# Kernel tuning notes

Hardware: AMD Instinct MI355X
Metric: run time of the kernel (lower is better)

Reference implementation:

```python
import jax, jax.numpy as jnp
import numpy as np
jax.config.update("jax_enable_x64", True)

N_ITER = 5
B, N = 64, 128

_C1 = jnp.uint64(0x9E3779B97F4A7C15)
_C2 = jnp.uint64(0xBF58476D1CE4E5B9)
_C3 = jnp.uint64(0x94D049BB133111EB)
_SALT = jnp.uint64(0xD1B54A32D192ED03)


def _mix(x):
    # splitmix64 finalizer: a bijection on uint64 -> preserves label equality classes
    z = x + _C1
    z = (z ^ (z >> jnp.uint64(30))) * _C2
    z = (z ^ (z >> jnp.uint64(27))) * _C3
    return z ^ (z >> jnp.uint64(31))


def setup_inputs() -> dict:
    key = jax.random.key(0)
    k1, k2 = jax.random.split(key)
    u = jax.random.uniform(k1, (B, N, N))
    adj = jnp.where(u < 0.06, 1.0, 0.0).astype(jnp.float32)
    adj = jnp.maximum(adj, jnp.transpose(adj, (0, 2, 1)))  # symmetric
    eye = jnp.eye(N, dtype=jnp.float32)
    adj = adj * (1.0 - eye)  # no self loops
    labels = jax.random.randint(k2, (B, N), 0, 10, dtype=jnp.int32)
    return {"adj": adj, "labels": labels}


def _kernel_contrib(h):
    # h: [B, N] uint64 labels. K[i,j] = #{(u,v): label_u == label_v}
    L = h.reshape(-1)                                   # [T]
    eq = (L[:, None] == L[None, :]).astype(jnp.float32)  # [T, T]
    return eq.reshape(B, N, B, N).sum(axis=(1, 3))       # [B, B]


def reference(adj, labels):
    adj_u = (adj > 0.5).astype(jnp.uint64)        # [B, N, N]
    h = _mix(labels.astype(jnp.uint64))           # initial labels (bijective relabel)
    K = _kernel_contrib(h)
    for _ in range(N_ITER):
        # commutative multiset hash of neighbor labels
        nsum = jnp.einsum('bij,bj->bi', adj_u, _mix(h ^ _SALT))
        # combine own label with neighbor multiset -> WL relabel
        h = _mix(_mix(h) + nsum)
        K = K + _kernel_contrib(h)
    d = jnp.sqrt(jnp.diag(K))
    return K / (d[:, None] * d[None, :])
```

## Files before the change

kernel.cpp:

```cpp
#include <hip/hip_runtime.h>

typedef unsigned long long u64;
typedef unsigned int u32;

#define NB 64
#define NN 128
#define NITER 5
#define NGEN 6
#define SALT 0xD1B54A32D192ED03ULL
#define NPAIR_OFF (NB*(NB-1)/2)
#define TSLOTS 256

__device__ __forceinline__ u64 mix64(u64 x) {
    u64 z = x + 0x9E3779B97F4A7C15ULL;
    z = (z ^ (z >> 30)) * 0xBF58476D1CE4E5B9ULL;
    z = (z ^ (z >> 27)) * 0x94D049BB133111EBULL;
    return z ^ (z >> 31);
}

__global__ __launch_bounds__(512) void wl_iter(const float* __restrict__ adj,
                                               const int* __restrict__ labels,
                                               u64* __restrict__ hgen,
                                               u32* __restrict__ KdiagU,
                                               float* __restrict__ out) {
    const int b = blockIdx.x;
    const int t = threadIdx.x;
    const int u = t & 127;
    const int q = t >> 7;

    __shared__ u64 gsh[NN];
    __shared__ u64 psum[3][NN];

    const float* rowp = adj + ((size_t)b * NN + u) * NN + q * 32;
    u32 m = 0;
    #pragma unroll
    for (int k = 0; k < 8; ++k) {
        const float4 v = *(const float4*)(rowp + 4 * k);
        m |= (v.x > 0.5f ? 1u : 0u) << (4 * k);
        m |= (v.y > 0.5f ? 1u : 0u) << (4 * k + 1);
        m |= (v.z > 0.5f ? 1u : 0u) << (4 * k + 2);
        m |= (v.w > 0.5f ? 1u : 0u) << (4 * k + 3);
    }

    u64 h = 0;
    if (q == 0) {
        h = mix64((u64)(u32)labels[b * NN + u]);
        hgen[((size_t)b * NGEN) * NN + u] = h;
        if (u == 0) out[b * NB + b] = 1.0f;
        if (u == 1) KdiagU[b] = 0u;
    }

    for (int it = 0; it < NITER; ++it) {
        if (q == 0) gsh[u] = mix64(h ^ SALT);
        __syncthreads();
        u64 s = 0;
        {
            u32 mm = m;
            const u64* gp = gsh + q * 32;
            while (mm) { int j = __builtin_ctz(mm); mm &= mm - 1; s += gp[j]; }
        }
        if (q) psum[q - 1][u] = s;
        __syncthreads();
        if (q == 0) {
            h = mix64(mix64(h) + s + psum[0][u] + psum[1][u] + psum[2][u]);
            hgen[((size_t)b * NGEN + (it + 1)) * NN + u] = h;
        }
    }
}

__global__ __launch_bounds__(128) void wl_tables(const u64* __restrict__ hgen,
                                                 u64* __restrict__ keysg,
                                                 u32* __restrict__ cntsg,
                                                 u32* __restrict__ KdiagU) {
    const int bg = blockIdx.x;
    const int t = threadIdx.x;

    __shared__ u64 keys[TSLOTS];
    __shared__ u32 cnts[TSLOTS];
    keys[t] = 0ULL; keys[t + 128] = 0ULL;
    cnts[t] = 0u;   cnts[t + 128] = 0u;
    __syncthreads();

    const u64 h = hgen[(size_t)bg * NN + t];
    u32 s = (u32)h & (TSLOTS - 1);
    for (;;) {
        u64 old = atomicCAS((unsigned long long*)&keys[s], 0ULL, h);
        if (old == 0ULL || old == h) { atomicAdd(&cnts[s], 1u); break; }
        s = (s + 1) & (TSLOTS - 1);
    }
    __syncthreads();

    u32 acc;
    {
        const u64 k0 = keys[t], k1 = keys[t + 128];
        const u32 c0 = cnts[t], c1 = cnts[t + 128];
        keysg[(size_t)bg * TSLOTS + t]       = k0;
        keysg[(size_t)bg * TSLOTS + t + 128] = k1;
        cntsg[(size_t)bg * TSLOTS + t]       = c0;
        cntsg[(size_t)bg * TSLOTS + t + 128] = c1;
        acc = c0 * c0 + c1 * c1;
    }
    #pragma unroll
    for (int off = 32; off > 0; off >>= 1) acc += __shfl_down(acc, off);
    __shared__ u32 part[2];
    if ((t & 63) == 0) part[t >> 6] = acc;
    __syncthreads();
    if (t == 0) atomicAdd(&KdiagU[bg / NGEN], part[0] + part[1]);
}

__global__ __launch_bounds__(256) void wl_pairs(const u64* __restrict__ hgen,
                                                const u64* __restrict__ keysg,
                                                const u32* __restrict__ cntsg,
                                                const u32* __restrict__ KdiagU,
                                                float* __restrict__ out) {
    const int p = blockIdx.x;
    int b1 = (int)((1.0f + sqrtf(1.0f + 8.0f * (float)p)) * 0.5f);
    while (b1 * (b1 - 1) / 2 > p) --b1;
    while ((b1 + 1) * b1 / 2 <= p) ++b1;
    const int b2 = p - b1 * (b1 - 1) / 2;

    const int t = threadIdx.x;
    __shared__ u64 keys[NGEN * TSLOTS];
    __shared__ u32 cnts[NGEN * TSLOTS];

    {
        const ulonglong2* src = (const ulonglong2*)(keysg + (size_t)b2 * NGEN * TSLOTS);
        ulonglong2* dst = (ulonglong2*)keys;
        #pragma unroll
        for (int k = 0; k < 3; ++k) dst[t + 256 * k] = src[t + 256 * k];
    }
    {
        const uint4* src = (const uint4*)(cntsg + (size_t)b2 * NGEN * TSLOTS);
        uint4* dst = (uint4*)cnts;
        #pragma unroll
        for (int k = 0; k < 2; ++k) {
            const int idx = t + 256 * k;
            if (idx < 384) dst[idx] = src[idx];
        }
    }
    __syncthreads();

    u32 c = 0;
    const u64* abase = hgen + (size_t)b1 * NGEN * NN;
    #pragma unroll
    for (int k = 0; k < 3; ++k) {
        const int idx = t + 256 * k;
        const u64 a = abase[idx];
        const int base = (idx >> 7) * TSLOTS;
        u32 s = (u32)a & (TSLOTS - 1);
        for (;;) {
            const u64 kk = keys[base + s];
            if (kk == a) { c += cnts[base + s]; break; }
            if (kk == 0ULL) break;
            s = (s + 1) & (TSLOTS - 1);
        }
    }

    #pragma unroll
    for (int off = 32; off > 0; off >>= 1) c += __shfl_down(c, off);
    __shared__ u32 part[4];
    if ((t & 63) == 0) part[t >> 6] = c;
    __syncthreads();
    if (t == 0) {
        const float v = (float)(part[0] + part[1] + part[2] + part[3])
                      / (sqrtf((float)KdiagU[b1]) * sqrtf((float)KdiagU[b2]));
        out[b1 * NB + b2] = v;
        out[b2 * NB + b1] = v;
    }
}

extern "C" void kernel_launch(void* const* d_in, const int* in_sizes, int n_in,
                              void* d_out, int out_size, void* d_ws, size_t ws_size,
                              hipStream_t stream) {
    const float* adj   = (const float*)d_in[0];
    const int*  labels = (const int*)d_in[1];
    float* out = (float*)d_out;

    char* ws = (char*)d_ws;
    u64* hgen  = (u64*)ws;
    u64* keysg = (u64*)(ws + 512 * 1024);
    u32* cntsg = (u32*)(ws + 1536 * 1024);
    u32* KdiagU = (u32*)(ws + 2048 * 1024);

    wl_iter  <<<NB, 512, 0, stream>>>(adj, labels, hgen, KdiagU, out);
    wl_tables<<<NB * NGEN, 128, 0, stream>>>(hgen, keysg, cntsg, KdiagU);
    wl_pairs <<<NPAIR_OFF, 256, 0, stream>>>(hgen, keysg, cntsg, KdiagU, out);
}
```

Before: 27.96 us.

## Fuse WL iteration and per-generation hash table build into one kernel

Merges the iteration kernel and the histogram-table kernel into one per-graph block that builds all six generation tables in shared memory, then writes them out and computes the diagonal norm directly. This drops a kernel launch and the global round-trip of hgen between the two stages, and removes the KdiagU atomics and zero-initialisation. The neighbour-sum step now runs on 128 threads with 64-bit masks instead of splitting across 512 threads, which serialises more work per thread and drops one barrier per iteration. Shared memory use per block rises to about 30 KB.

```diff
diff --git a/kernel.cpp b/kernel.cpp
--- a/kernel.cpp
+++ b/kernel.cpp
@@ -18,100 +18,117 @@
     return z ^ (z >> 31);
 }
 
-__global__ __launch_bounds__(512) void wl_iter(const float* __restrict__ adj,
-                                               const int* __restrict__ labels,
-                                               u64* __restrict__ hgen,
-                                               u32* __restrict__ KdiagU,
-                                               float* __restrict__ out) {
+__global__ __launch_bounds__(512) void wl_build(const float* __restrict__ adj,
+                                                const int* __restrict__ labels,
+                                                u64* __restrict__ hgen,
+                                                u64* __restrict__ keysg,
+                                                u32* __restrict__ cntsg,
+                                                float* __restrict__ Kdiag,
+                                                float* __restrict__ out) {
     const int b = blockIdx.x;
     const int t = threadIdx.x;
     const int u = t & 127;
     const int q = t >> 7;
 
-    __shared__ u64 gsh[NN];
-    __shared__ u64 psum[3][NN];
-
-    const float* rowp = adj + ((size_t)b * NN + u) * NN + q * 32;
-    u32 m = 0;
-    #pragma unroll
-    for (int k = 0; k < 8; ++k) {
-        const float4 v = *(const float4*)(rowp + 4 * k);
-        m |= (v.x > 0.5f ? 1u : 0u) << (4 * k);
-        m |= (v.y > 0.5f ? 1u : 0u) << (4 * k + 1);
-        m |= (v.z > 0.5f ? 1u : 0u) << (4 * k + 2);
-        m |= (v.w > 0.5f ? 1u : 0u) << (4 * k + 3);
-    }
-
-    u64 h = 0;
-    if (q == 0) {
+    __shared__ u32 bits[4][NN];
+    __shared__ u64 gsh[2][NN];
+    __shared__ u64 hall[NGEN][NN];
+    __shared__ u64 keys[NGEN*TSLOTS];
+    __shared__ u32 cnts[NGEN*TSLOTS];
+    __shared__ u32 part[8];
+
+    {
+        const float* rowp = adj + ((size_t)b * NN + u) * NN + q * 32;
+        u32 m = 0;
+        #pragma unroll
+        for (int k = 0; k < 8; ++k) {
+            const float4 v = *(const float4*)(rowp + 4 * k);
+            m |= (v.x > 0.5f ? 1u : 0u) << (4 * k);
+            m |= (v.y > 0.5f ? 1u : 0u) << (4 * k + 1);
+            m |= (v.z > 0.5f ? 1u : 0u) << (4 * k + 2);
+            m |= (v.w > 0.5f ? 1u : 0u) << (4 * k + 3);
+        }
+        bits[q][u] = m;
+    }
+    #pragma unroll
+    for (int k = 0; k < 3; ++k) { keys[t + 512 * k] = 0ULL; cnts[t + 512 * k] = 0u; }
+    __syncthreads();
+
+    u64 h = 0, mA = 0, mB = 0;
+    if (t < NN) {
+        mA = (u64)bits[0][u] | ((u64)bits[1][u] << 32);
+        mB = (u64)bits[2][u] | ((u64)bits[3][u] << 32);
         h = mix64((u64)(u32)labels[b * NN + u]);
-        hgen[((size_t)b * NGEN) * NN + u] = h;
-        if (u == 0) out[b * NB + b] = 1.0f;
-        if (u == 1) KdiagU[b] = 0u;
-    }
-
+        hall[0][u] = h;
+        hgen[(size_t)b * (NGEN * NN) + u] = h;
+    }
     for (int it = 0; it < NITER; ++it) {
-        if (q == 0) gsh[u] = mix64(h ^ SALT);
+        if (t < NN) gsh[it & 1][u] = mix64(h ^ SALT);
         __syncthreads();
-        u64 s = 0;
-        {
-            u32 mm = m;
-            const u64* gp = gsh + q * 32;
-            while (mm) { int j = __builtin_ctz(mm); mm &= mm - 1; s += gp[j]; }
-        }
-        if (q) psum[q - 1][u] = s;
-        __syncthreads();
-        if (q == 0) {
-            h = mix64(mix64(h) + s + psum[0][u] + psum[1][u] + psum[2][u]);
-            hgen[((size_t)b * NGEN + (it + 1)) * NN + u] = h;
-        }
-    }
-}
-
-__global__ __launch_bounds__(128) void wl_tables(const u64* __restrict__ hgen,
-                                                 u64* __restrict__ keysg,
-                                                 u32* __restrict__ cntsg,
-                                                 u32* __restrict__ KdiagU) {
-    const int bg = blockIdx.x;
-    const int t = threadIdx.x;
-
-    __shared__ u64 keys[TSLOTS];
-    __shared__ u32 cnts[TSLOTS];
-    keys[t] = 0ULL; keys[t + 128] = 0ULL;
-    cnts[t] = 0u;   cnts[t + 128] = 0u;
-    __syncthreads();
-
-    const u64 h = hgen[(size_t)bg * NN + t];
-    u32 s = (u32)h & (TSLOTS - 1);
-    for (;;) {
-        u64 old = atomicCAS((unsigned long long*)&keys[s], 0ULL, h);
-        if (old == 0ULL || old == h) { atomicAdd(&cnts[s], 1u); break; }
-        s = (s + 1) & (TSLOTS - 1);
-    }
-    __syncthreads();
-
-    u32 acc;
-    {
-        const u64 k0 = keys[t], k1 = keys[t + 128];
-        const u32 c0 = cnts[t], c1 = cnts[t + 128];
-        keysg[(size_t)bg * TSLOTS + t]       = k0;
-        keysg[(size_t)bg * TSLOTS + t + 128] = k1;
-        cntsg[(size_t)bg * TSLOTS + t]       = c0;
-        cntsg[(size_t)bg * TSLOTS + t + 128] = c1;
-        acc = c0 * c0 + c1 * c1;
+        if (t < NN) {
+            const u64* gp = gsh[it & 1];
+            u64 s = 0;
+            u64 mm = mA;
+            while (mm) { int j = __builtin_ctzll(mm); mm &= mm - 1; s += gp[j]; }
+            mm = mB;
+            while (mm) { int j = __builtin_ctzll(mm); mm &= mm - 1; s += gp[64 + j]; }
+            h = mix64(mix64(h) + s);
+            hall[it + 1][u] = h;
+            hgen[(size_t)b * (NGEN * NN) + (it + 1) * NN + u] = h;
+        }
+    }
+    __syncthreads();
+
+    {
+        const u64 key = hall[t >> 7][u];
+        u32 s = ((u32)key & (TSLOTS - 1)) + (t >> 7) * TSLOTS;
+        const u32 base = (t >> 7) * TSLOTS;
+        for (;;) {
+            u64 old = atomicCAS((unsigned long long*)&keys[s], 0ULL, key);
+            if (old == 0ULL || old == key) { atomicAdd(&cnts[s], 1u); break; }
+            s = base + ((s + 1) & (TSLOTS - 1));
+        }
+    }
+    if (t < 256) {
+        const int gen = 4 + (t >> 7);
+        const u64 key = hall[gen][u];
+        const u32 base = gen * TSLOTS;
+        u32 s = ((u32)key & (TSLOTS - 1)) + base;
+        for (;;) {
+            u64 old = atomicCAS((unsigned long long*)&keys[s], 0ULL, key);
+            if (old == 0ULL || old == key) { atomicAdd(&cnts[s], 1u); break; }
+            s = base + ((s + 1) & (TSLOTS - 1));
+        }
+    }
+    __syncthreads();
+
+    u32 acc = 0;
+    #pragma unroll
+    for (int k = 0; k < 3; ++k) {
+        const int idx = t + 512 * k;
+        const u64 kk = keys[idx];
+        const u32 cc = cnts[idx];
+        keysg[(size_t)b * (NGEN * TSLOTS) + idx] = kk;
+        cntsg[(size_t)b * (NGEN * TSLOTS) + idx] = cc;
+        acc += cc * cc;
     }
     #pragma unroll
     for (int off = 32; off > 0; off >>= 1) acc += __shfl_down(acc, off);
-    __shared__ u32 part[2];
     if ((t & 63) == 0) part[t >> 6] = acc;
     __syncthreads();
-    if (t == 0) atomicAdd(&KdiagU[bg / NGEN], part[0] + part[1]);
+    if (t == 0) {
+        u32 d = 0;
+        #pragma unroll
+        for (int w = 0; w < 8; ++w) d += part[w];
+        Kdiag[b] = sqrtf((float)d);
+        out[b * NB + b] = 1.0f;
+    }
 }
 
 __global__ __launch_bounds__(256) void wl_pairs(const u64* __restrict__ hgen,
                                                 const u64* __restrict__ keysg,
                                                 const u32* __restrict__ cntsg,
-                                                const u32* __restrict__ KdiagU,
+                                                const float* __restrict__ Kdiag,
                                                 float* __restrict__ out) {
     const int p = blockIdx.x;
     int b1 = (int)((1.0f + sqrtf(1.0f + 8.0f * (float)p)) * 0.5f);
@@ -163,7 +180,7 @@
     __syncthreads();
     if (t == 0) {
         const float v = (float)(part[0] + part[1] + part[2] + part[3])
-                      / (sqrtf((float)KdiagU[b1]) * sqrtf((float)KdiagU[b2]));
+                      / (Kdiag[b1] * Kdiag[b2]);
         out[b1 * NB + b2] = v;
         out[b2 * NB + b1] = v;
     }
@@ -177,12 +194,11 @@
     float* out = (float*)d_out;
 
     char* ws = (char*)d_ws;
-    u64* hgen  = (u64*)ws;
-    u64* keysg = (u64*)(ws + 512 * 1024);
-    u32* cntsg = (u32*)(ws + 1536 * 1024);
-    u32* KdiagU = (u32*)(ws + 2048 * 1024);
-
-    wl_iter  <<<NB, 512, 0, stream>>>(adj, labels, hgen, KdiagU, out);
-    wl_tables<<<NB * NGEN, 128, 0, stream>>>(hgen, keysg, cntsg, KdiagU);
-    wl_pairs <<<NPAIR_OFF, 256, 0, stream>>>(hgen, keysg, cntsg, KdiagU, out);
-}
+    u64*   hgen  = (u64*)ws;
+    u64*   keysg = (u64*)(ws + 512 * 1024);
+    u32*   cntsg = (u32*)(ws + 1536 * 1024);
+    float* Kdiag = (float*)(ws + 2048 * 1024);
+
+    wl_build<<<NB, 512, 0, stream>>>(adj, labels, hgen, keysg, cntsg, Kdiag, out);
+    wl_pairs<<<NPAIR_OFF, 256, 0, stream>>>(hgen, keysg, cntsg, Kdiag, out);
+}
```

After: 31.51 us. +12.7%, slower.

## Run WL relabel iterations in a single wavefront using ballot and shuffles

Applied to the files above, without the earlier changes.

Replaces the 512-thread WL iteration kernel with a 64-lane one-wavefront-per-graph kernel. Adjacency bitmasks are built with __ballot over rows, and neighbor sums gather labels via __shfl, so there is no shared memory and no __syncthreads. This removes block-level barriers and the partial-sum reduction. The cost is much less parallelism for loading adjacency: 128 serial row iterations per wave, and each lane handles two nodes. It also moves KdiagU in the workspace layout.

```diff
diff --git a/kernel.cpp b/kernel.cpp
--- a/kernel.cpp
+++ b/kernel.cpp
@@ -18,54 +18,47 @@
     return z ^ (z >> 31);
 }
 
-__global__ __launch_bounds__(512) void wl_iter(const float* __restrict__ adj,
-                                               const int* __restrict__ labels,
-                                               u64* __restrict__ hgen,
-                                               u32* __restrict__ KdiagU,
-                                               float* __restrict__ out) {
+__global__ __launch_bounds__(64) void wl_iter_wave(const float* __restrict__ adj,
+                                                   const int* __restrict__ labels,
+                                                   u64* __restrict__ hgen,
+                                                   u32* __restrict__ KdiagU,
+                                                   float* __restrict__ out) {
     const int b = blockIdx.x;
-    const int t = threadIdx.x;
-    const int u = t & 127;
-    const int q = t >> 7;
+    const int lane = threadIdx.x;
 
-    __shared__ u64 gsh[NN];
-    __shared__ u64 psum[3][NN];
-
-    const float* rowp = adj + ((size_t)b * NN + u) * NN + q * 32;
-    u32 m = 0;
-    #pragma unroll
-    for (int k = 0; k < 8; ++k) {
-        const float4 v = *(const float4*)(rowp + 4 * k);
-        m |= (v.x > 0.5f ? 1u : 0u) << (4 * k);
-        m |= (v.y > 0.5f ? 1u : 0u) << (4 * k + 1);
-        m |= (v.z > 0.5f ? 1u : 0u) << (4 * k + 2);
-        m |= (v.w > 0.5f ? 1u : 0u) << (4 * k + 3);
+    const float* abase = adj + (size_t)b * NN * NN;
+    u64 mA0 = 0, mA1 = 0, mB0 = 0, mB1 = 0;
+    #pragma unroll 8
+    for (int k = 0; k < NN; ++k) {
+        const float* arow = abase + (size_t)k * NN;
+        const u64 m0 = __ballot(arow[lane] > 0.5f);
+        const u64 m1 = __ballot(arow[64 + lane] > 0.5f);
+        if (k == lane)      { mA0 = m0; mA1 = m1; }
+        if (k == lane + 64) { mB0 = m0; mB1 = m1; }
     }
 
-    u64 h = 0;
-    if (q == 0) {
-        h = mix64((u64)(u32)labels[b * NN + u]);
-        hgen[((size_t)b * NGEN) * NN + u] = h;
-        if (u == 0) out[b * NB + b] = 1.0f;
-        if (u == 1) KdiagU[b] = 0u;
+    u64 h0 = mix64((u64)(u32)labels[b * NN + lane]);
+    u64 h1 = mix64((u64)(u32)labels[b * NN + 64 + lane]);
+    u64* hg = hgen + (size_t)b * (NGEN * NN);
+    hg[lane] = h0;
+    hg[64 + lane] = h1;
+
+    for (int it = 0; it < NITER; ++it) {
+        const u64 g0 = mix64(h0 ^ SALT);
+        const u64 g1 = mix64(h1 ^ SALT);
+        u64 s0 = 0, s1 = 0, m;
+        m = mA0; while (m) { int j = __builtin_ctzll(m); m &= m - 1; s0 += (u64)__shfl((long long)g0, j); }
+        m = mA1; while (m) { int j = __builtin_ctzll(m); m &= m - 1; s0 += (u64)__shfl((long long)g1, j); }
+        m = mB0; while (m) { int j = __builtin_ctzll(m); m &= m - 1; s1 += (u64)__shfl((long long)g0, j); }
+        m = mB1; while (m) { int j = __builtin_ctzll(m); m &= m - 1; s1 += (u64)__shfl((long long)g1, j); }
+        h0 = mix64(mix64(h0) + s0);
+        h1 = mix64(mix64(h1) + s1);
+        hg += NN;
+        hg[lane] = h0;
+        hg[64 + lane] = h1;
     }
 
-    for (int it = 0; it < NITER; ++it) {
-        if (q == 0) gsh[u] = mix64(h ^ SALT);
-        __syncthreads();
-        u64 s = 0;
-        {
-            u32 mm = m;
-            const u64* gp = gsh + q * 32;
-            while (mm) { int j = __builtin_ctz(mm); mm &= mm - 1; s += gp[j]; }
-        }
-        if (q) psum[q - 1][u] = s;
-        __syncthreads();
-        if (q == 0) {
-            h = mix64(mix64(h) + s + psum[0][u] + psum[1][u] + psum[2][u]);
-            hgen[((size_t)b * NGEN + (it + 1)) * NN + u] = h;
-        }
-    }
+    if (lane == 0) { KdiagU[b] = 0u; out[b * NB + b] = 1.0f; }
 }
 
 __global__ __launch_bounds__(128) void wl_tables(const u64* __restrict__ hgen,
@@ -177,12 +170,12 @@
     float* out = (float*)d_out;
 
     char* ws = (char*)d_ws;
-    u64* hgen  = (u64*)ws;
-    u64* keysg = (u64*)(ws + 512 * 1024);
-    u32* cntsg = (u32*)(ws + 1536 * 1024);
-    u32* KdiagU = (u32*)(ws + 2048 * 1024);
+    u64* hgen   = (u64*)ws;
+    u32* KdiagU = (u32*)(ws + 448 * 1024);
+    u64* keysg  = (u64*)(ws + 512 * 1024);
+    u32* cntsg  = (u32*)(ws + 1536 * 1024);
 
-    wl_iter  <<<NB, 512, 0, stream>>>(adj, labels, hgen, KdiagU, out);
-    wl_tables<<<NB * NGEN, 128, 0, stream>>>(hgen, keysg, cntsg, KdiagU);
-    wl_pairs <<<NPAIR_OFF, 256, 0, stream>>>(hgen, keysg, cntsg, KdiagU, out);
+    wl_iter_wave<<<NB, 64, 0, stream>>>(adj, labels, hgen, KdiagU, out);
+    wl_tables   <<<NB * NGEN, 128, 0, stream>>>(hgen, keysg, cntsg, KdiagU);
+    wl_pairs    <<<NPAIR_OFF, 256, 0, stream>>>(hgen, keysg, cntsg, KdiagU, out);
 }
```

Measured after the change: 47.23 us. 1.69x slower.

## Fuse WL iteration and hash-table build into one kernel via redundant recompute

Applied to the files above, without the earlier changes.

Merges the iteration and table-building kernels into one launch. Extra blocks each recompute the WL labels up to their own generation and then build that generation's hash table, so no dependency on hgen written by another block is needed. The per-graph diagonal is stored as per-generation partial floats and summed in the pairs kernel, which removes the global atomic and the zero-init. This saves one kernel launch and one global round trip, at the cost of redundant label recomputation and extra adjacency reads in the table blocks.

```diff
diff --git a/kernel.cpp b/kernel.cpp
--- a/kernel.cpp
+++ b/kernel.cpp
@@ -18,39 +18,47 @@
     return z ^ (z >> 31);
 }
 
-__global__ __launch_bounds__(512) void wl_iter(const float* __restrict__ adj,
-                                               const int* __restrict__ labels,
-                                               u64* __restrict__ hgen,
-                                               u32* __restrict__ KdiagU,
-                                               float* __restrict__ out) {
-    const int b = blockIdx.x;
+__global__ __launch_bounds__(512) void wl_stage1(const float* __restrict__ adj,
+                                                 const int* __restrict__ labels,
+                                                 u64* __restrict__ hgen,
+                                                 u64* __restrict__ keysg,
+                                                 u32* __restrict__ cntsg,
+                                                 float* __restrict__ Kpart,
+                                                 float* __restrict__ out) {
+    const int blk = blockIdx.x;
     const int t = threadIdx.x;
     const int u = t & 127;
     const int q = t >> 7;
+    const bool writer = blk < NB;
+    const int b    = writer ? blk   : (blk - NB) / NGEN;
+    const int gent = writer ? NITER : (blk - NB) % NGEN;
 
     __shared__ u64 gsh[NN];
     __shared__ u64 psum[3][NN];
+    __shared__ u64 keys[TSLOTS];
+    __shared__ u32 cnts[TSLOTS];
+    __shared__ u32 part[4];
 
-    const float* rowp = adj + ((size_t)b * NN + u) * NN + q * 32;
     u32 m = 0;
-    #pragma unroll
-    for (int k = 0; k < 8; ++k) {
-        const float4 v = *(const float4*)(rowp + 4 * k);
-        m |= (v.x > 0.5f ? 1u : 0u) << (4 * k);
-        m |= (v.y > 0.5f ? 1u : 0u) << (4 * k + 1);
-        m |= (v.z > 0.5f ? 1u : 0u) << (4 * k + 2);
-        m |= (v.w > 0.5f ? 1u : 0u) << (4 * k + 3);
+    if (gent > 0) {
+        const float* rowp = adj + ((size_t)b * NN + u) * NN + q * 32;
+        #pragma unroll
+        for (int k = 0; k < 8; ++k) {
+            const float4 v = *(const float4*)(rowp + 4 * k);
+            m |= (v.x > 0.5f ? 1u : 0u) << (4 * k);
+            m |= (v.y > 0.5f ? 1u : 0u) << (4 * k + 1);
+            m |= (v.z > 0.5f ? 1u : 0u) << (4 * k + 2);
+            m |= (v.w > 0.5f ? 1u : 0u) << (4 * k + 3);
+        }
     }
 
     u64 h = 0;
     if (q == 0) {
         h = mix64((u64)(u32)labels[b * NN + u]);
-        hgen[((size_t)b * NGEN) * NN + u] = h;
-        if (u == 0) out[b * NB + b] = 1.0f;
-        if (u == 1) KdiagU[b] = 0u;
+        if (writer) hgen[(size_t)b * (NGEN * NN) + u] = h;
     }
 
-    for (int it = 0; it < NITER; ++it) {
+    for (int it = 0; it < gent; ++it) {
         if (q == 0) gsh[u] = mix64(h ^ SALT);
         __syncthreads();
         u64 s = 0;
@@ -63,55 +71,45 @@
         __syncthreads();
         if (q == 0) {
             h = mix64(mix64(h) + s + psum[0][u] + psum[1][u] + psum[2][u]);
-            hgen[((size_t)b * NGEN + (it + 1)) * NN + u] = h;
+            if (writer) hgen[(size_t)b * (NGEN * NN) + (it + 1) * NN + u] = h;
         }
     }
-}
+    if (writer) return;
 
-__global__ __launch_bounds__(128) void wl_tables(const u64* __restrict__ hgen,
-                                                 u64* __restrict__ keysg,
-                                                 u32* __restrict__ cntsg,
-                                                 u32* __restrict__ KdiagU) {
-    const int bg = blockIdx.x;
-    const int t = threadIdx.x;
-
-    __shared__ u64 keys[TSLOTS];
-    __shared__ u32 cnts[TSLOTS];
-    keys[t] = 0ULL; keys[t + 128] = 0ULL;
-    cnts[t] = 0u;   cnts[t + 128] = 0u;
+    if (t < TSLOTS) { keys[t] = 0ULL; cnts[t] = 0u; }
     __syncthreads();
-
-    const u64 h = hgen[(size_t)bg * NN + t];
-    u32 s = (u32)h & (TSLOTS - 1);
-    for (;;) {
-        u64 old = atomicCAS((unsigned long long*)&keys[s], 0ULL, h);
-        if (old == 0ULL || old == h) { atomicAdd(&cnts[s], 1u); break; }
-        s = (s + 1) & (TSLOTS - 1);
+    if (q == 0) {
+        u32 s = (u32)h & (TSLOTS - 1);
+        for (;;) {
+            u64 old = atomicCAS((unsigned long long*)&keys[s], 0ULL, h);
+            if (old == 0ULL || old == h) { atomicAdd(&cnts[s], 1u); break; }
+            s = (s + 1) & (TSLOTS - 1);
+        }
     }
     __syncthreads();
 
-    u32 acc;
-    {
-        const u64 k0 = keys[t], k1 = keys[t + 128];
-        const u32 c0 = cnts[t], c1 = cnts[t + 128];
-        keysg[(size_t)bg * TSLOTS + t]       = k0;
-        keysg[(size_t)bg * TSLOTS + t + 128] = k1;
-        cntsg[(size_t)bg * TSLOTS + t]       = c0;
-        cntsg[(size_t)bg * TSLOTS + t + 128] = c1;
-        acc = c0 * c0 + c1 * c1;
+    const int bg = b * NGEN + gent;
+    if (t < TSLOTS) {
+        const u64 kk = keys[t];
+        const u32 cc = cnts[t];
+        keysg[(size_t)bg * TSLOTS + t] = kk;
+        cntsg[(size_t)bg * TSLOTS + t] = cc;
+        u32 acc = cc * cc;
+        #pragma unroll
+        for (int off = 32; off > 0; off >>= 1) acc += __shfl_down(acc, off);
+        if ((t & 63) == 0) part[t >> 6] = acc;
     }
-    #pragma unroll
-    for (int off = 32; off > 0; off >>= 1) acc += __shfl_down(acc, off);
-    __shared__ u32 part[2];
-    if ((t & 63) == 0) part[t >> 6] = acc;
     __syncthreads();
-    if (t == 0) atomicAdd(&KdiagU[bg / NGEN], part[0] + part[1]);
+    if (t == 0) {
+        Kpart[bg] = (float)(part[0] + part[1] + part[2] + part[3]);
+        if (gent == 0) out[b * NB + b] = 1.0f;
+    }
 }
 
 __global__ __launch_bounds__(256) void wl_pairs(const u64* __restrict__ hgen,
                                                 const u64* __restrict__ keysg,
                                                 const u32* __restrict__ cntsg,
-                                                const u32* __restrict__ KdiagU,
+                                                const float* __restrict__ Kpart,
                                                 float* __restrict__ out) {
     const int p = blockIdx.x;
     int b1 = (int)((1.0f + sqrtf(1.0f + 8.0f * (float)p)) * 0.5f);
@@ -122,6 +120,11 @@
     const int t = threadIdx.x;
     __shared__ u64 keys[NGEN * TSLOTS];
     __shared__ u32 cnts[NGEN * TSLOTS];
+    __shared__ u32 part[4];
+    __shared__ float dred[2 * NGEN];
+
+    if (t < 2 * NGEN)
+        dred[t] = Kpart[(t < NGEN ? b1 : b2) * NGEN + (t % NGEN)];
 
     {
         const ulonglong2* src = (const ulonglong2*)(keysg + (size_t)b2 * NGEN * TSLOTS);
@@ -158,12 +161,14 @@
 
     #pragma unroll
     for (int off = 32; off > 0; off >>= 1) c += __shfl_down(c, off);
-    __shared__ u32 part[4];
     if ((t & 63) == 0) part[t >> 6] = c;
     __syncthreads();
     if (t == 0) {
+        float d1 = 0.f, d2 = 0.f;
+        #pragma unroll
+        for (int g = 0; g < NGEN; ++g) { d1 += dred[g]; d2 += dred[NGEN + g]; }
         const float v = (float)(part[0] + part[1] + part[2] + part[3])
-                      / (sqrtf((float)KdiagU[b1]) * sqrtf((float)KdiagU[b2]));
+                      / (sqrtf(d1) * sqrtf(d2));
         out[b1 * NB + b2] = v;
         out[b2 * NB + b1] = v;
     }
@@ -177,12 +182,12 @@
     float* out = (float*)d_out;
 
     char* ws = (char*)d_ws;
-    u64* hgen  = (u64*)ws;
-    u64* keysg = (u64*)(ws + 512 * 1024);
-    u32* cntsg = (u32*)(ws + 1536 * 1024);
-    u32* KdiagU = (u32*)(ws + 2048 * 1024);
+    u64*   hgen  = (u64*)ws;
+    float* Kpart = (float*)(ws + 448 * 1024);
+    u64*   keysg = (u64*)(ws + 512 * 1024);
+    u32*   cntsg = (u32*)(ws + 1536 * 1024);
 
-    wl_iter  <<<NB, 512, 0, stream>>>(adj, labels, hgen, KdiagU, out);
-    wl_tables<<<NB * NGEN, 128, 0, stream>>>(hgen, keysg, cntsg, KdiagU);
-    wl_pairs <<<NPAIR_OFF, 256, 0, stream>>>(hgen, keysg, cntsg, KdiagU, out);
+    wl_stage1<<<NB + NB * NGEN, 512, 0, stream>>>(adj, labels, hgen, keysg,
+                                                  cntsg, Kpart, out);
+    wl_pairs <<<NPAIR_OFF, 256, 0, stream>>>(hgen, keysg, cntsg, Kpart, out);
 }
```

Result: no change. 27.86 us (-0.4%).
